# Optimization experiments

Measured on AMD Instinct MI355X. Metric: run time of the kernel, lower is better.

Reference implementation:

```python
import jax, jax.numpy as jnp
import numpy as np

B, N = 16, 16          # batch, boxes per image
H, W = 640, 640        # image size
PH, PW = 300, 300      # learned patch size
MIN_AREA = 60.0
MAX_ANG = 20.0 * np.pi / 180.0


def setup_inputs() -> dict:
    key = jax.random.key(0)
    k1, k2, k3 = jax.random.split(key, 3)
    images = jax.random.uniform(k1, (B, H, W, 3), jnp.float32, -1.0, 1.0)
    patch = jax.random.uniform(k2, (PH, PW, 3), jnp.float32, -1.0, 1.0)
    kb1, kb2, kb3 = jax.random.split(k3, 3)
    ymin = jax.random.uniform(kb1, (B, N), jnp.float32, 0.0, H - 220.0)
    xmin = jax.random.uniform(kb2, (B, N), jnp.float32, 0.0, W - 220.0)
    hw = jax.random.uniform(kb3, (B, N, 2), jnp.float32, 100.0, 200.0)
    boxes = jnp.stack([ymin, xmin, ymin + hw[..., 0], xmin + hw[..., 1]], axis=-1)
    scale = jnp.float32(0.4)
    return {"boxes": boxes, "images": images, "patch": patch, "scale": scale}


def _bilinear(img, ys, xs):
    # img [Ph,Pw,3]; ys,xs [H,W] continuous source coords -> [H,W,3]
    Ph, Pw = img.shape[0], img.shape[1]
    y0 = jnp.floor(ys)
    x0 = jnp.floor(xs)
    wy = (ys - y0)[..., None]
    wx = (xs - x0)[..., None]
    y0i = jnp.clip(y0.astype(jnp.int32), 0, Ph - 1)
    y1i = jnp.clip(y0i + 1, 0, Ph - 1)
    x0i = jnp.clip(x0.astype(jnp.int32), 0, Pw - 1)
    x1i = jnp.clip(x0i + 1, 0, Pw - 1)
    v00 = img[y0i, x0i]
    v01 = img[y0i, x1i]
    v10 = img[y1i, x0i]
    v11 = img[y1i, x1i]
    return v00 * (1 - wy) * (1 - wx) + v01 * (1 - wy) * wx + v10 * wy * (1 - wx) + v11 * wy * wx


def _per_image(img, boxes_i, patch, scale, key):
    # random_print_adjust: per-channel affine jitter of the patch
    kw, kb, kloop = jax.random.split(key, 3)
    w = jax.random.normal(kw, (1, 1, 3), jnp.float32) * 0.1 + 0.5
    b = jax.random.normal(kb, (1, 1, 3), jnp.float32) * 0.01
    p = jnp.clip(w * patch + b, -1.0, 1.0)
    # BrightnessMatcher: shift patch mean brightness to match the image
    p = jnp.clip(p + (jnp.mean(img) - jnp.mean(p)), -1.0, 1.0)

    oimg = img
    mask0 = jnp.zeros_like(img)
    yy, xx = jnp.meshgrid(jnp.arange(H, dtype=jnp.float32),
                          jnp.arange(W, dtype=jnp.float32), indexing="ij")

    def step(carry, inp):
        image, mask = carry
        box, kk = inp
        ymin, xmin, ymax, xmax = box[0], box[1], box[2], box[3]
        h = ymax - ymin
        ww = xmax - xmin
        longer = jnp.maximum(h, ww)
        ps = jnp.floor(longer * scale)                       # patch_h == patch_w
        diag = jnp.minimum(jnp.sqrt(2.0).astype(jnp.float32) * ps, jnp.float32(W))
        oy = ymin + h / 2.0
        ox = xmin + ww / 2.0
        y0 = jnp.maximum(oy - diag / 2.0, 0.0)
        x0 = jnp.maximum(ox - diag / 2.0, 0.0)
        y0 = jnp.where(y0 + diag > H, H - diag, y0)
        x0 = jnp.where(x0 + diag > W, W - diag, x0)
        # int casts as in the TF code (values are >= 0, trunc == floor)
        y0i = jnp.floor(y0)
        x0i = jnp.floor(x0)
        phi = jnp.maximum(jnp.floor(ps), 1.0)
        diagi = jnp.floor(diag)
        valid_box = (phi * phi) > MIN_AREA

        k1, k2, k3 = jax.random.split(kk, 3)
        angle = jax.random.uniform(k1, (), jnp.float32, -MAX_ANG, MAX_ANG)

        # inverse warp: output pixel -> padded-patch coords -> resized-patch coords
        u = yy - y0i
        v = xx - x0i
        in_sq = (u >= 0) & (v >= 0) & (u < diagi) & (v < diagi)
        c = (diagi - 1.0) / 2.0
        ca, sa = jnp.cos(angle), jnp.sin(angle)
        su = c + ca * (u - c) - sa * (v - c)
        sv = c + sa * (u - c) + ca * (v - c)
        top = jnp.floor((diagi - phi) / 2.0)   # pad offset (floor top/left)
        py = su - top
        px = sv - top
        valid_src = (py >= 0) & (py <= phi - 1) & (px >= 0) & (px <= phi - 1)
        # resized-patch coords -> original patch coords (bilinear resize, half-pixel)
        sy = (py + 0.5) * (PH / phi) - 0.5
        sx = (px + 0.5) * (PW / phi) - 0.5
        samp = _bilinear(p, sy, sx)                                   # [H,W,3]
        noise = jax.random.uniform(k2, samp.shape, jnp.float32, -0.1, 0.1)
        bright = jax.random.uniform(k3, (), jnp.float32, -0.3, 0.3)
        im = jnp.clip(samp + noise + bright, -1.0, 1.0)
        val = jnp.where(valid_src[..., None], im, -2.0)
        val = jnp.where(val < -1.0, image, val)   # fill with current background
        val = jnp.clip(val, -1.0, 1.0)
        sel = (in_sq & valid_box)[..., None]
        new_image = jnp.where(sel, val, image)
        new_mask = jnp.where(sel, oimg - val, mask)
        return (new_image, new_mask), None

    keys = jax.random.split(kloop, N)
    (img_out, mask_out), _ = jax.lax.scan(step, (img, mask0), (boxes_i, keys))
    return img_out, mask_out


def reference(boxes, images, patch, scale):
    keys = jax.random.split(jax.random.key(42), B)
    img_out, mask_out = jax.vmap(_per_image, in_axes=(0, 0, None, None, 0))(
        images, boxes, patch, scale, keys)
    return img_out, mask_out
```

## Files before the change

### kernel.cpp

```cpp
#include <hip/hip_runtime.h>
#include <stdint.h>
#include <math.h>

#define B_ 16
#define N_ 16
#define H_ 640
#define W_ 640
#define PH_ 300
#define PW_ 300

#define IMG_ELEMS (H_*W_*3)
#define PATCH_ELEMS (PH_*PW_*3)

__device__ __forceinline__ uint2 tf2x32(uint32_t k0, uint32_t k1, uint32_t x0, uint32_t x1) {
  uint32_t k2 = k0 ^ k1 ^ 0x1BD11BDAu;
#define TFR(r) x0 += x1; x1 = (x1 << (r)) | (x1 >> (32 - (r))); x1 ^= x0;
  x0 += k0; x1 += k1;
  TFR(13) TFR(15) TFR(26) TFR(6)
  x0 += k1; x1 += k2 + 1u;
  TFR(17) TFR(29) TFR(16) TFR(24)
  x0 += k2; x1 += k0 + 2u;
  TFR(13) TFR(15) TFR(26) TFR(6)
  x0 += k0; x1 += k1 + 3u;
  TFR(17) TFR(29) TFR(16) TFR(24)
  x0 += k1; x1 += k2 + 4u;
  TFR(13) TFR(15) TFR(26) TFR(6)
  x0 += k2; x1 += k0 + 5u;
#undef TFR
  return make_uint2(x0, x1);
}

__device__ __forceinline__ uint32_t rb32(uint32_t k0, uint32_t k1, uint32_t i) {
  uint2 o = tf2x32(k0, k1, 0u, i);
  return o.x ^ o.y;
}

__device__ __forceinline__ float u01f(uint32_t bits) {
  return __uint_as_float((bits >> 9) | 0x3F800000u) - 1.0f;
}

__device__ __forceinline__ float erfinv32(float x) {
  float w = -log1pf(-x * x);
  float p;
  if (w < 5.0f) {
    w = w - 2.5f;
    p = 2.81022636e-08f;
    p = fmaf(p, w, 3.43273939e-07f);
    p = fmaf(p, w, -3.5233877e-06f);
    p = fmaf(p, w, -4.39150654e-06f);
    p = fmaf(p, w, 0.00021858087f);
    p = fmaf(p, w, -0.00125372503f);
    p = fmaf(p, w, -0.00417768164f);
    p = fmaf(p, w, 0.246640727f);
    p = fmaf(p, w, 1.50140941f);
  } else {
    w = sqrtf(w) - 3.0f;
    p = -0.000200214257f;
    p = fmaf(p, w, 0.000100950558f);
    p = fmaf(p, w, 0.00134934322f);
    p = fmaf(p, w, -0.00367342844f);
    p = fmaf(p, w, 0.00573950773f);
    p = fmaf(p, w, -0.0076224613f);
    p = fmaf(p, w, 0.00943887047f);
    p = fmaf(p, w, 1.00167406f);
    p = fmaf(p, w, 2.83297682f);
  }
  return p * x;
}

__device__ __forceinline__ float jnormal(uint32_t bits) {
  float lo = __uint_as_float(0xBF7FFFFFu);
  float span = 1.0f - lo;
  float u = fmaxf(lo, u01f(bits) * span + lo);
  return 1.4142135623730951f * erfinv32(u);
}

__global__ void setup_kernel(const float* __restrict__ boxes, const float* __restrict__ scale_p,
                             float* __restrict__ params, float* __restrict__ wb) {
  int t = threadIdx.x;
  if (t >= B_*N_) return;
  int b = t >> 4, n = t & 15;
  uint2 kb = tf2x32(0u, 42u, 0u, (uint32_t)b);
  uint2 kw  = tf2x32(kb.x, kb.y, 0u, 0u);
  uint2 kbk = tf2x32(kb.x, kb.y, 0u, 1u);
  uint2 kl  = tf2x32(kb.x, kb.y, 0u, 2u);
  if (n == 0) {
    wb[b*8+0] = jnormal(rb32(kw.x,  kw.y,  0u)) * 0.1f + 0.5f;
    wb[b*8+1] = jnormal(rb32(kw.x,  kw.y,  1u)) * 0.1f + 0.5f;
    wb[b*8+2] = jnormal(rb32(kw.x,  kw.y,  2u)) * 0.1f + 0.5f;
    wb[b*8+3] = jnormal(rb32(kbk.x, kbk.y, 0u)) * 0.01f;
    wb[b*8+4] = jnormal(rb32(kbk.x, kbk.y, 1u)) * 0.01f;
    wb[b*8+5] = jnormal(rb32(kbk.x, kbk.y, 2u)) * 0.01f;
  }
  uint2 kk = tf2x32(kl.x, kl.y, 0u, (uint32_t)n);
  uint2 k1 = tf2x32(kk.x, kk.y, 0u, 0u);
  uint2 k2 = tf2x32(kk.x, kk.y, 0u, 1u);
  uint2 k3 = tf2x32(kk.x, kk.y, 0u, 2u);
  const float MA = (float)(20.0 * 3.14159265358979323846 / 180.0);
  float angle  = fmaxf(-MA,   u01f(rb32(k1.x, k1.y, 0u)) * (MA - (-MA)) + (-MA));
  float bright = fmaxf(-0.3f, u01f(rb32(k3.x, k3.y, 0u)) * (0.3f - (-0.3f)) + (-0.3f));

  const float* bx = boxes + (size_t)t * 4;
  float ymin = bx[0], xmin = bx[1], ymax = bx[2], xmax = bx[3];
  float sc = scale_p[0];
  float h = ymax - ymin, ww = xmax - xmin;
  float longer = fmaxf(h, ww);
  float ps = floorf(longer * sc);
  float diag = fminf(sqrtf(2.0f) * ps, (float)W_);
  float oy = ymin + h * 0.5f;
  float ox = xmin + ww * 0.5f;
  float y0 = fmaxf(oy - diag * 0.5f, 0.0f);
  float x0 = fmaxf(ox - diag * 0.5f, 0.0f);
  if (y0 + diag > (float)H_) y0 = (float)H_ - diag;
  if (x0 + diag > (float)W_) x0 = (float)W_ - diag;
  float y0i = floorf(y0), x0i = floorf(x0);
  float phi = fmaxf(floorf(ps), 1.0f);
  float diagi = floorf(diag);
  float validf = ((phi * phi) > 60.0f) ? 1.0f : 0.0f;
  float c = (diagi - 1.0f) * 0.5f;
  float top = floorf((diagi - phi) * 0.5f);

  float* P = params + t * 16;
  P[0] = y0i; P[1] = x0i; P[2] = diagi; P[3] = phi;
  P[4] = c;
  P[5] = (float)cos((double)angle);
  P[6] = (float)sin((double)angle);
  P[7] = top;
  P[8] = bright; P[9] = (float)PH_ / phi; P[10] = 0.0f; P[11] = validf;
  P[12] = __uint_as_float(k2.x); P[13] = __uint_as_float(k2.y); P[14] = 0.0f; P[15] = 0.0f;
}

__global__ __launch_bounds__(256) void reduce_kernel(
    const float* __restrict__ images, const float* __restrict__ patch,
    const float* __restrict__ wb, double* __restrict__ partials) {
  int b = blockIdx.y, j = blockIdx.x, t = threadIdx.x;
  const float* img = images + (size_t)b * IMG_ELEMS;
  double s = 0.0;
  for (int i = j * 256 + t; i < IMG_ELEMS; i += 64 * 256) s += (double)img[i];
  float w0 = wb[b*8+0], w1 = wb[b*8+1], w2 = wb[b*8+2];
  float b0 = wb[b*8+3], b1 = wb[b*8+4], b2 = wb[b*8+5];
  double sp = 0.0;
  for (int i = j * 256 + t; i < PATCH_ELEMS; i += 64 * 256) {
    int q = i / 3; int ch = i - q * 3;
    float wv = (ch == 0) ? w0 : ((ch == 1) ? w1 : w2);
    float bv = (ch == 0) ? b0 : ((ch == 1) ? b1 : b2);
    float pv = fminf(fmaxf(wv * patch[i] + bv, -1.0f), 1.0f);
    sp += (double)pv;
  }
  __shared__ double sh[256];
  sh[t] = s; __syncthreads();
  for (int o = 128; o > 0; o >>= 1) { if (t < o) sh[t] += sh[t + o]; __syncthreads(); }
  if (t == 0) partials[((size_t)b * 64 + j) * 2 + 0] = sh[0];
  __syncthreads();
  sh[t] = sp; __syncthreads();
  for (int o = 128; o > 0; o >>= 1) { if (t < o) sh[t] += sh[t + o]; __syncthreads(); }
  if (t == 0) partials[((size_t)b * 64 + j) * 2 + 1] = sh[0];
}

__global__ void finalize_kernel(const double* __restrict__ partials, float* __restrict__ dvals) {
  int t = threadIdx.x;
  if (t < B_) {
    double si = 0.0, sp = 0.0;
    for (int j = 0; j < 64; j++) {
      si += partials[((size_t)t * 64 + j) * 2 + 0];
      sp += partials[((size_t)t * 64 + j) * 2 + 1];
    }
    float mi = (float)(si / (double)IMG_ELEMS);
    float mp = (float)(sp / (double)PATCH_ELEMS);
    dvals[t] = mi - mp;
  }
}

__global__ __launch_bounds__(256) void main_kernel(
    const float* __restrict__ images, const float* __restrict__ patch,
    const float* __restrict__ params, const float* __restrict__ wb,
    const float* __restrict__ dvals, float* __restrict__ out) {
  __shared__ float sP[N_ * 16];
  __shared__ float sWB[6];
  __shared__ float sD;
  int b = blockIdx.y;
  int tid = threadIdx.x;
  if (tid < N_ * 16) sP[tid] = params[b * N_ * 16 + tid];
  if (tid < 6) sWB[tid] = wb[b * 8 + tid];
  if (tid == 0) sD = dvals[b];
  __syncthreads();
  int p = blockIdx.x * 256 + tid;
  int y = p / W_;
  int x = p - y * W_;
  size_t base = ((size_t)b * (H_ * W_) + (size_t)p) * 3;
  float orig[3], img[3], mk[3];
#pragma unroll
  for (int ch = 0; ch < 3; ch++) { orig[ch] = images[base + ch]; img[ch] = orig[ch]; mk[ch] = 0.0f; }
  float yf = (float)y, xf = (float)x;
  float dsh = sD;
  for (int n = 0; n < N_; n++) {
    const float* P = sP + n * 16;
    if (P[11] == 0.0f) continue;
    float u = yf - P[0];
    float v = xf - P[1];
    float diagi = P[2];
    if (!(u >= 0.0f && v >= 0.0f && u < diagi && v < diagi)) continue;
    float phi = P[3], c = P[4], ca = P[5], sa = P[6], top = P[7], bright = P[8], sph = P[9];
    float t1 = u - c, t2 = v - c;
    float su = c + ca * t1 - sa * t2;
    float sv = c + sa * t1 + ca * t2;
    float py = su - top;
    float px = sv - top;
    bool vsrc = (py >= 0.0f) && (py <= phi - 1.0f) && (px >= 0.0f) && (px <= phi - 1.0f);
    if (vsrc) {
      float sy = (py + 0.5f) * sph - 0.5f;
      float sx = (px + 0.5f) * sph - 0.5f;
      float fy = floorf(sy), fx = floorf(sx);
      float wy = sy - fy, wxv = sx - fx;
      int iy0 = min(max((int)fy, 0), PH_ - 1);
      int iy1 = min(iy0 + 1, PH_ - 1);
      int ix0 = min(max((int)fx, 0), PW_ - 1);
      int ix1 = min(ix0 + 1, PW_ - 1);
      int o00 = (iy0 * PW_ + ix0) * 3;
      int o01 = (iy0 * PW_ + ix1) * 3;
      int o10 = (iy1 * PW_ + ix0) * 3;
      int o11 = (iy1 * PW_ + ix1) * 3;
      uint32_t k2a = __float_as_uint(P[12]);
      uint32_t k2b = __float_as_uint(P[13]);
      float omwy = 1.0f - wy, omwx = 1.0f - wxv;
      int nbase = p * 3;
#pragma unroll
      for (int ch = 0; ch < 3; ch++) {
        float wv = sWB[ch], bv = sWB[3 + ch];
        float a00 = fminf(fmaxf(wv * patch[o00 + ch] + bv, -1.0f), 1.0f);
        float a01 = fminf(fmaxf(wv * patch[o01 + ch] + bv, -1.0f), 1.0f);
        float a10 = fminf(fmaxf(wv * patch[o10 + ch] + bv, -1.0f), 1.0f);
        float a11 = fminf(fmaxf(wv * patch[o11 + ch] + bv, -1.0f), 1.0f);
        a00 = fminf(fmaxf(a00 + dsh, -1.0f), 1.0f);
        a01 = fminf(fmaxf(a01 + dsh, -1.0f), 1.0f);
        a10 = fminf(fmaxf(a10 + dsh, -1.0f), 1.0f);
        a11 = fminf(fmaxf(a11 + dsh, -1.0f), 1.0f);
        float samp = ((a00 * omwy) * omwx) + ((a01 * omwy) * wxv)
                   + ((a10 * wy) * omwx) + ((a11 * wy) * wxv);
        int i = nbase + ch;
        uint32_t bits = rb32(k2a, k2b, (uint32_t)i);
        float nz = fmaxf(-0.1f, u01f(bits) * (0.1f - (-0.1f)) + (-0.1f));
        float imv = fminf(fmaxf((samp + nz) + bright, -1.0f), 1.0f);
        img[ch] = imv;
        mk[ch] = orig[ch] - imv;
      }
    } else {
#pragma unroll
      for (int ch = 0; ch < 3; ch++) mk[ch] = orig[ch] - img[ch];
    }
  }
  size_t moff = (size_t)B_ * (H_ * W_) * 3;
#pragma unroll
  for (int ch = 0; ch < 3; ch++) {
    out[base + ch] = img[ch];
    out[moff + base + ch] = mk[ch];
  }
}

extern "C" void kernel_launch(void* const* d_in, const int* in_sizes, int n_in,
                              void* d_out, int out_size, void* d_ws, size_t ws_size,
                              hipStream_t stream) {
  const float* boxes  = (const float*)d_in[0];
  const float* images = (const float*)d_in[1];
  const float* patch  = (const float*)d_in[2];
  const float* scale  = (const float*)d_in[3];
  float* out = (float*)d_out;

  float* params = (float*)d_ws;
  float* wb     = params + B_ * N_ * 16;
  float* dvals  = wb + B_ * 8;
  double* partials = (double*)((char*)d_ws + 20480);

  setup_kernel<<<1, 256, 0, stream>>>(boxes, scale, params, wb);
  reduce_kernel<<<dim3(64, B_), 256, 0, stream>>>(images, patch, wb, partials);
  finalize_kernel<<<1, 64, 0, stream>>>(partials, dvals);
  main_kernel<<<dim3((H_ * W_) / 256, B_), 256, 0, stream>>>(images, patch, params, wb, dvals, out);
}
```

Measured before the change: 302.6 us.

## Fuse finalize into main kernel, process 4 pixels per thread with box culling

Drops the separate finalize kernel: each main-kernel block now reduces the 64 partial sums itself. Each thread handles 4 consecutive pixels using vectorized 16-byte loads and nontemporal stores. A per-block list of boxes whose rows overlap the block's pixel range is built so threads skip boxes that cannot touch them. This removes one launch and some redundant per-pixel box tests, in exchange for more register pressure and fewer blocks in flight.

```diff
diff --git a/kernel.cpp b/kernel.cpp
--- a/kernel.cpp
+++ b/kernel.cpp
@@ -11,6 +11,8 @@
 
 #define IMG_ELEMS (H_*W_*3)
 #define PATCH_ELEMS (PH_*PW_*3)
+
+typedef float f32x4 __attribute__((ext_vector_type(4)));
 
 __device__ __forceinline__ uint2 tf2x32(uint32_t k0, uint32_t k1, uint32_t x0, uint32_t x1) {
   uint32_t k2 = k0 ^ k1 ^ 0x1BD11BDAu;
@@ -157,104 +159,143 @@
   if (t == 0) partials[((size_t)b * 64 + j) * 2 + 1] = sh[0];
 }
 
-__global__ void finalize_kernel(const double* __restrict__ partials, float* __restrict__ dvals) {
-  int t = threadIdx.x;
-  if (t < B_) {
-    double si = 0.0, sp = 0.0;
-    for (int j = 0; j < 64; j++) {
-      si += partials[((size_t)t * 64 + j) * 2 + 0];
-      sp += partials[((size_t)t * 64 + j) * 2 + 1];
-    }
-    float mi = (float)(si / (double)IMG_ELEMS);
-    float mp = (float)(sp / (double)PATCH_ELEMS);
-    dvals[t] = mi - mp;
-  }
-}
-
 __global__ __launch_bounds__(256) void main_kernel(
     const float* __restrict__ images, const float* __restrict__ patch,
     const float* __restrict__ params, const float* __restrict__ wb,
-    const float* __restrict__ dvals, float* __restrict__ out) {
+    const double* __restrict__ partials, float* __restrict__ out) {
   __shared__ float sP[N_ * 16];
   __shared__ float sWB[6];
   __shared__ float sD;
+  __shared__ int sList[N_];
+  __shared__ int sCount;
+  __shared__ double sRi[64], sRp[64];
+
   int b = blockIdx.y;
   int tid = threadIdx.x;
   if (tid < N_ * 16) sP[tid] = params[b * N_ * 16 + tid];
   if (tid < 6) sWB[tid] = wb[b * 8 + tid];
-  if (tid == 0) sD = dvals[b];
+  if (tid < 64) {
+    sRi[tid] = partials[((size_t)b * 64 + tid) * 2 + 0];
+    sRp[tid] = partials[((size_t)b * 64 + tid) * 2 + 1];
+  }
   __syncthreads();
-  int p = blockIdx.x * 256 + tid;
-  int y = p / W_;
-  int x = p - y * W_;
-  size_t base = ((size_t)b * (H_ * W_) + (size_t)p) * 3;
-  float orig[3], img[3], mk[3];
+  if (tid == 0) {
+    double si = 0.0, sp = 0.0;
+    for (int j = 0; j < 64; j++) { si += sRi[j]; sp += sRp[j]; }
+    float mi = (float)(si / (double)IMG_ELEMS);
+    float mp = (float)(sp / (double)PATCH_ELEMS);
+    sD = mi - mp;
+    int pblk = blockIdx.x * 1024;
+    int ys = pblk / W_;
+    int ye = (pblk + 1023) / W_;
+    int cnt = 0;
+    for (int n = 0; n < N_; n++) {
+      const float* P = sP + n * 16;
+      if (P[11] == 0.0f) continue;
+      float fy0 = P[0];
+      float fy1 = P[0] + P[2] - 1.0f;
+      if (fy1 < (float)ys || fy0 > (float)ye) continue;
+      sList[cnt++] = n;
+    }
+    sCount = cnt;
+  }
+  __syncthreads();
+
+  int g = blockIdx.x * 256 + tid;
+  int p0 = g * 4;
+  int y = p0 / W_;
+  int x0 = p0 - y * W_;
+  size_t base = ((size_t)b * (H_ * W_) + (size_t)p0) * 3;
+
+  const f32x4* iv = (const f32x4*)(images + base);
+  f32x4 q0 = iv[0], q1 = iv[1], q2 = iv[2];
+  float orig[12] = {q0.x, q0.y, q0.z, q0.w, q1.x, q1.y, q1.z, q1.w, q2.x, q2.y, q2.z, q2.w};
+  float img[12], mk[12];
 #pragma unroll
-  for (int ch = 0; ch < 3; ch++) { orig[ch] = images[base + ch]; img[ch] = orig[ch]; mk[ch] = 0.0f; }
-  float yf = (float)y, xf = (float)x;
+  for (int e = 0; e < 12; e++) { img[e] = orig[e]; mk[e] = 0.0f; }
+
+  float yf = (float)y;
   float dsh = sD;
-  for (int n = 0; n < N_; n++) {
+  int cnt = sCount;
+  for (int li = 0; li < cnt; li++) {
+    int n = sList[li];
     const float* P = sP + n * 16;
-    if (P[11] == 0.0f) continue;
+    float diagi = P[2];
     float u = yf - P[0];
-    float v = xf - P[1];
-    float diagi = P[2];
-    if (!(u >= 0.0f && v >= 0.0f && u < diagi && v < diagi)) continue;
+    if (!(u >= 0.0f && u < diagi)) continue;
     float phi = P[3], c = P[4], ca = P[5], sa = P[6], top = P[7], bright = P[8], sph = P[9];
-    float t1 = u - c, t2 = v - c;
-    float su = c + ca * t1 - sa * t2;
-    float sv = c + sa * t1 + ca * t2;
-    float py = su - top;
-    float px = sv - top;
-    bool vsrc = (py >= 0.0f) && (py <= phi - 1.0f) && (px >= 0.0f) && (px <= phi - 1.0f);
-    if (vsrc) {
-      float sy = (py + 0.5f) * sph - 0.5f;
-      float sx = (px + 0.5f) * sph - 0.5f;
-      float fy = floorf(sy), fx = floorf(sx);
-      float wy = sy - fy, wxv = sx - fx;
-      int iy0 = min(max((int)fy, 0), PH_ - 1);
-      int iy1 = min(iy0 + 1, PH_ - 1);
-      int ix0 = min(max((int)fx, 0), PW_ - 1);
-      int ix1 = min(ix0 + 1, PW_ - 1);
-      int o00 = (iy0 * PW_ + ix0) * 3;
-      int o01 = (iy0 * PW_ + ix1) * 3;
-      int o10 = (iy1 * PW_ + ix0) * 3;
-      int o11 = (iy1 * PW_ + ix1) * 3;
-      uint32_t k2a = __float_as_uint(P[12]);
-      uint32_t k2b = __float_as_uint(P[13]);
-      float omwy = 1.0f - wy, omwx = 1.0f - wxv;
-      int nbase = p * 3;
+    uint32_t k2a = __float_as_uint(P[12]);
+    uint32_t k2b = __float_as_uint(P[13]);
+    float t1 = u - c;
+    float cct1 = c + ca * t1;
+    float cst1 = c + sa * t1;
 #pragma unroll
-      for (int ch = 0; ch < 3; ch++) {
-        float wv = sWB[ch], bv = sWB[3 + ch];
-        float a00 = fminf(fmaxf(wv * patch[o00 + ch] + bv, -1.0f), 1.0f);
-        float a01 = fminf(fmaxf(wv * patch[o01 + ch] + bv, -1.0f), 1.0f);
-        float a10 = fminf(fmaxf(wv * patch[o10 + ch] + bv, -1.0f), 1.0f);
-        float a11 = fminf(fmaxf(wv * patch[o11 + ch] + bv, -1.0f), 1.0f);
-        a00 = fminf(fmaxf(a00 + dsh, -1.0f), 1.0f);
-        a01 = fminf(fmaxf(a01 + dsh, -1.0f), 1.0f);
-        a10 = fminf(fmaxf(a10 + dsh, -1.0f), 1.0f);
-        a11 = fminf(fmaxf(a11 + dsh, -1.0f), 1.0f);
-        float samp = ((a00 * omwy) * omwx) + ((a01 * omwy) * wxv)
-                   + ((a10 * wy) * omwx) + ((a11 * wy) * wxv);
-        int i = nbase + ch;
-        uint32_t bits = rb32(k2a, k2b, (uint32_t)i);
-        float nz = fmaxf(-0.1f, u01f(bits) * (0.1f - (-0.1f)) + (-0.1f));
-        float imv = fminf(fmaxf((samp + nz) + bright, -1.0f), 1.0f);
-        img[ch] = imv;
-        mk[ch] = orig[ch] - imv;
+    for (int j = 0; j < 4; j++) {
+      float v = (float)(x0 + j) - P[1];
+      if (!(v >= 0.0f && v < diagi)) continue;
+      float t2 = v - c;
+      float su = cct1 - sa * t2;
+      float sv = cst1 + ca * t2;
+      float py = su - top;
+      float px = sv - top;
+      bool vsrc = (py >= 0.0f) && (py <= phi - 1.0f) && (px >= 0.0f) && (px <= phi - 1.0f);
+      if (vsrc) {
+        float sy = (py + 0.5f) * sph - 0.5f;
+        float sx = (px + 0.5f) * sph - 0.5f;
+        float fy = floorf(sy), fx = floorf(sx);
+        float wy = sy - fy, wxv = sx - fx;
+        int iy0 = min(max((int)fy, 0), PH_ - 1);
+        int iy1 = min(iy0 + 1, PH_ - 1);
+        int ix0 = min(max((int)fx, 0), PW_ - 1);
+        int ix1 = min(ix0 + 1, PW_ - 1);
+        int o00 = (iy0 * PW_ + ix0) * 3;
+        int o01 = (iy0 * PW_ + ix1) * 3;
+        int o10 = (iy1 * PW_ + ix0) * 3;
+        int o11 = (iy1 * PW_ + ix1) * 3;
+        float omwy = 1.0f - wy, omwx = 1.0f - wxv;
+        int nbase = (p0 + j) * 3;
+#pragma unroll
+        for (int ch = 0; ch < 3; ch++) {
+          float wv = sWB[ch], bv = sWB[3 + ch];
+          float a00 = fminf(fmaxf(wv * patch[o00 + ch] + bv, -1.0f), 1.0f);
+          float a01 = fminf(fmaxf(wv * patch[o01 + ch] + bv, -1.0f), 1.0f);
+          float a10 = fminf(fmaxf(wv * patch[o10 + ch] + bv, -1.0f), 1.0f);
+          float a11 = fminf(fmaxf(wv * patch[o11 + ch] + bv, -1.0f), 1.0f);
+          a00 = fminf(fmaxf(a00 + dsh, -1.0f), 1.0f);
+          a01 = fminf(fmaxf(a01 + dsh, -1.0f), 1.0f);
+          a10 = fminf(fmaxf(a10 + dsh, -1.0f), 1.0f);
+          a11 = fminf(fmaxf(a11 + dsh, -1.0f), 1.0f);
+          float samp = ((a00 * omwy) * omwx) + ((a01 * omwy) * wxv)
+                     + ((a10 * wy) * omwx) + ((a11 * wy) * wxv);
+          int i = nbase + ch;
+          uint32_t bits = rb32(k2a, k2b, (uint32_t)i);
+          float nz = fmaxf(-0.1f, u01f(bits) * (0.1f - (-0.1f)) + (-0.1f));
+          float imv = fminf(fmaxf((samp + nz) + bright, -1.0f), 1.0f);
+          img[j * 3 + ch] = imv;
+          mk[j * 3 + ch] = orig[j * 3 + ch] - imv;
+        }
+      } else {
+#pragma unroll
+        for (int ch = 0; ch < 3; ch++) mk[j * 3 + ch] = orig[j * 3 + ch] - img[j * 3 + ch];
       }
-    } else {
-#pragma unroll
-      for (int ch = 0; ch < 3; ch++) mk[ch] = orig[ch] - img[ch];
     }
   }
+
   size_t moff = (size_t)B_ * (H_ * W_) * 3;
-#pragma unroll
-  for (int ch = 0; ch < 3; ch++) {
-    out[base + ch] = img[ch];
-    out[moff + base + ch] = mk[ch];
-  }
+  f32x4* ov = (f32x4*)(out + base);
+  f32x4* mv = (f32x4*)(out + moff + base);
+  f32x4 o0 = {img[0], img[1], img[2],  img[3]};
+  f32x4 o1 = {img[4], img[5], img[6],  img[7]};
+  f32x4 o2 = {img[8], img[9], img[10], img[11]};
+  f32x4 m0 = {mk[0],  mk[1],  mk[2],   mk[3]};
+  f32x4 m1 = {mk[4],  mk[5],  mk[6],   mk[7]};
+  f32x4 m2 = {mk[8],  mk[9],  mk[10],  mk[11]};
+  __builtin_nontemporal_store(o0, ov + 0);
+  __builtin_nontemporal_store(o1, ov + 1);
+  __builtin_nontemporal_store(o2, ov + 2);
+  __builtin_nontemporal_store(m0, mv + 0);
+  __builtin_nontemporal_store(m1, mv + 1);
+  __builtin_nontemporal_store(m2, mv + 2);
 }
 
 extern "C" void kernel_launch(void* const* d_in, const int* in_sizes, int n_in,
@@ -268,11 +309,9 @@
 
   float* params = (float*)d_ws;
   float* wb     = params + B_ * N_ * 16;
-  float* dvals  = wb + B_ * 8;
   double* partials = (double*)((char*)d_ws + 20480);
 
   setup_kernel<<<1, 256, 0, stream>>>(boxes, scale, params, wb);
   reduce_kernel<<<dim3(64, B_), 256, 0, stream>>>(images, patch, wb, partials);
-  finalize_kernel<<<1, 64, 0, stream>>>(partials, dvals);
-  main_kernel<<<dim3((H_ * W_) / 256, B_), 256, 0, stream>>>(images, patch, params, wb, dvals, out);
-}
+  main_kernel<<<dim3((H_ * W_) / 1024, B_), 256, 0, stream>>>(images, patch, params, wb, partials, out);
+}
```

Result: slower. 337.5 us (+11.5%).
